# Kernel optimization log

Measured on AMD Instinct MI355X. Metric: run time of the kernel, lower is better.

Reference implementation:

```python
import jax, jax.numpy as jnp
import numpy as np
from jax import lax

STRIDE = 1
PADDING = 4
Q = 5


def setup_inputs() -> dict:
    key = jax.random.key(0)
    k1, k2, k3 = jax.random.split(key, 3)
    B, C_in, T = 16, 128, 8192
    C_out, K = 256, 9
    x = jax.random.normal(k1, (B, C_in, T), dtype=jnp.float32)
    fan_in = C_in * K
    std = np.sqrt(2.0 / fan_in).astype(np.float32)
    conv_weights = jax.random.normal(k2, (C_out, C_in, K, Q), dtype=jnp.float32) * std
    # init matches _initialize_weights' operator_probs pattern plus small noise
    operator_probs = jnp.concatenate(
        [jnp.full((C_out, 1), 1.5), jnp.full((C_out, Q - 1), 0.25)], axis=1
    ) + 0.01 * jax.random.normal(k3, (C_out, Q), dtype=jnp.float32)
    return {"x": x, "conv_weights": conv_weights, "operator_probs": operator_probs}


def _selfonn_forward(x, conv_weights, operator_probs):
    # Fuse the q parallel convs into one conv with q*C_out output channels.
    C_out, C_in, K, q = conv_weights.shape
    # (O, I, K, q) -> (q, O, I, K) -> (q*O, I, K); q-major output channel order
    w = jnp.transpose(conv_weights, (3, 0, 1, 2)).reshape(q * C_out, C_in, K)
    z = lax.conv_general_dilated(
        x, w,
        window_strides=(STRIDE,),
        padding=[(PADDING, PADDING)],
        dimension_numbers=("NCH", "OIH", "NCH"),
    )  # (B, q*C_out, T_out)
    B = x.shape[0]
    T_out = z.shape[-1]
    z = z.reshape(B, q, C_out, T_out)
    # per-branch nonlinearities: identity, sin, cos, tanh, clamped exp
    outs = jnp.stack(
        [
            z[:, 0],
            jnp.sin(z[:, 1]),
            jnp.cos(z[:, 2]),
            jnp.tanh(z[:, 3]),
            jnp.exp(jnp.clip(z[:, 4], -8.0, 8.0)),
        ],
        axis=-1,
    )  # (B, C_out, T_out, q)
    op_w = jax.nn.softmax(operator_probs, axis=1)  # (C_out, q)
    return jnp.einsum("bctq,cq->bct", outs, op_w)


def reference(x, conv_weights, operator_probs):
    return _selfonn_forward(x, conv_weights, operator_probs)
```

## Files before the change

### kernel.cpp

```cpp
#include <hip/hip_runtime.h>

#define CI   128
#define TT   8192
#define CO   256
#define KW   9
#define NQ   5
#define PADL 4
#define KDIM (CI*KW)
#define NSTEP (KDIM/32)
#define NCHUNK (NSTEP/2)
#define NF (NQ*NCHUNK)
#define BCO  128
#define BT   128
#define XROWS 136
#define XPITCH 136

typedef __attribute__((ext_vector_type(8))) short short8;
typedef __attribute__((ext_vector_type(4))) float float4v;
typedef __attribute__((address_space(1))) const unsigned int ga_u32;
typedef __attribute__((address_space(3))) unsigned int la_u32;

static __device__ __forceinline__ short f2bf(float f) {
  union { float f; unsigned u; } c; c.f = f;
  unsigned u = c.u;
  unsigned r = (u + 0x7FFFu + ((u >> 16) & 1u)) >> 16;
  return (short)r;
}

static __device__ __forceinline__ float tanh_fast(float z) {
  float e = __expf(2.f * z);
  return (e - 1.f) / (e + 1.f);
}

static __device__ __forceinline__ void gload_lds16(const void* g, void* l) {
  __builtin_amdgcn_global_load_lds((ga_u32*)g, (la_u32*)l, 16, 0, 0);
}

__global__ void selfonn_wtrans(const float* __restrict__ w, short* __restrict__ wT, int n) {
  int o = blockIdx.x * 256 + threadIdx.x;
  if (o >= n) return;
  int ci = o & (CI - 1);
  int k  = (o >> 7) % KW;
  int co = (o / KDIM) & (CO - 1);
  int q  = o / (KDIM * CO);
  wT[o] = f2bf(w[((co * CI + ci) * KW + k) * NQ + q]);
}

__global__ __launch_bounds__(256, 2) void selfonn_main(
    const float* __restrict__ x, const short* __restrict__ wT,
    const float* __restrict__ probs, float* __restrict__ out) {

  __shared__ __align__(16) short xs[XROWS][XPITCH];
  __shared__ __align__(16) short ws[2][2][BCO][32];
  __shared__ float opw[BCO][NQ];

  const int tid  = threadIdx.x;
  const int lane = tid & 63;
  const int wid  = tid >> 6;
  const int wm   = wid >> 1;
  const int wn   = wid & 1;
  const int l15  = lane & 15;
  const int lg   = lane >> 4;
  const int b    = blockIdx.z;
  const int co0  = blockIdx.y * BCO;
  const int t0   = blockIdx.x * BT;

  if (tid < BCO) {
    float p[NQ];
    float mx = -1e30f;
    #pragma unroll
    for (int j = 0; j < NQ; ++j) { p[j] = probs[(co0 + tid) * NQ + j]; mx = fmaxf(mx, p[j]); }
    float s = 0.f;
    #pragma unroll
    for (int j = 0; j < NQ; ++j) { p[j] = __expf(p[j] - mx); s += p[j]; }
    float inv = 1.0f / s;
    #pragma unroll
    for (int j = 0; j < NQ; ++j) opw[tid][j] = p[j] * inv;
  }

  const float* xb = x + (size_t)b * CI * TT;
  #pragma unroll
  for (int it = 0; it < 17; ++it) {
    int cell = tid + it * 256;
    int ci = cell & (CI - 1);
    int tc = cell >> 7;
    int tg = t0 - PADL + tc * 4;
    float4v v = {0.f, 0.f, 0.f, 0.f};
    if (tg >= 0 && tg <= TT - 4)
      v = *(const float4v*)(xb + (size_t)ci * TT + tg);
    int tl = tc * 4;
    xs[tl + 0][ci] = f2bf(v[0]);
    xs[tl + 1][ci] = f2bf(v[1]);
    xs[tl + 2][ci] = f2bf(v[2]);
    xs[tl + 3][ci] = f2bf(v[3]);
  }

  auto stage = [&](int fi, int buf) {
    int q     = fi / NCHUNK;
    int chunk = fi - q * NCHUNK;
    const short* wqp = wT + ((size_t)q * CO + co0) * KDIM + chunk * 64;
    short* lb = &ws[buf][0][0][0];
    #pragma unroll
    for (int r = 0; r < 4; ++r) {
      int idx_l = r * 256 + tid;
      int sc    = idx_l >> 9;
      int rem   = idx_l & 511;
      int co_l  = rem >> 2;
      int part  = rem & 3;
      const short* src = wqp + (size_t)co_l * KDIM + sc * 32 + part * 8;
      gload_lds16(src, lb + (size_t)(r * 256 + wid * 64) * 8);
    }
  };

  float4v oacc[4][4];
  float4v acc[4][4];
  #pragma unroll
  for (int m = 0; m < 4; ++m)
    #pragma unroll
    for (int n = 0; n < 4; ++n) {
      oacc[m][n] = (float4v){0.f, 0.f, 0.f, 0.f};
      acc[m][n]  = (float4v){0.f, 0.f, 0.f, 0.f};
    }

  stage(0, 0);
  __syncthreads();

  int cur = 0;
  for (int fi = 0; fi < NF; ++fi) {
    if (fi + 1 < NF) stage(fi + 1, cur ^ 1);

    int q     = fi / NCHUNK;
    int chunk = fi - q * NCHUNK;

    #pragma unroll
    for (int sc = 0; sc < 2; ++sc) {
      int step = chunk * 2 + sc;
      int k    = step >> 2;
      int ci0  = (step & 3) * 32;
      short8 af[4], bfv[4];
      #pragma unroll
      for (int m = 0; m < 4; ++m)
        af[m] = *(const short8*)&ws[cur][sc][wm * 64 + m * 16 + l15][8 * lg];
      #pragma unroll
      for (int n = 0; n < 4; ++n)
        bfv[n] = *(const short8*)&xs[wn * 64 + n * 16 + l15 + k][ci0 + 8 * lg];
      #pragma unroll
      for (int m = 0; m < 4; ++m)
        #pragma unroll
        for (int n = 0; n < 4; ++n)
          acc[m][n] = __builtin_amdgcn_mfma_f32_16x16x32_bf16(af[m], bfv[n], acc[m][n], 0, 0, 0);
    }

    if (chunk == NCHUNK - 1) {
      #define DO_EPI(FEXPR)                                            \
        _Pragma("unroll") for (int m = 0; m < 4; ++m) {                \
          _Pragma("unroll") for (int jj = 0; jj < 4; ++jj) {           \
            int co_l = wm * 64 + m * 16 + lg * 4 + jj;                 \
            float wqv = opw[co_l][q];                                  \
            _Pragma("unroll") for (int n = 0; n < 4; ++n) {            \
              float z = acc[m][n][jj];                                 \
              float f = (FEXPR);                                       \
              oacc[m][n][jj] += wqv * f;                               \
              acc[m][n][jj] = 0.f;                                     \
            }                                                          \
          }                                                            \
        }
      if (q == 0)      { DO_EPI(z) }
      else if (q == 1) { DO_EPI(__sinf(z)) }
      else if (q == 2) { DO_EPI(__cosf(z)) }
      else if (q == 3) { DO_EPI(tanh_fast(z)) }
      else             { DO_EPI(__expf(fminf(fmaxf(z, -8.f), 8.f))) }
      #undef DO_EPI
    }

    __syncthreads();
    cur ^= 1;
  }

  float* ob = out + (size_t)(b * CO + co0) * TT;
  #pragma unroll
  for (int m = 0; m < 4; ++m) {
    #pragma unroll
    for (int jj = 0; jj < 4; ++jj) {
      int co_l = wm * 64 + m * 16 + lg * 4 + jj;
      int tcol = t0 + wn * 64 + l15;
      float* orow = ob + (size_t)co_l * TT + tcol;
      #pragma unroll
      for (int n = 0; n < 4; ++n)
        orow[n * 16] = oacc[m][n][jj];
    }
  }
}

extern "C" void kernel_launch(void* const* d_in, const int* in_sizes, int n_in,
                              void* d_out, int out_size, void* d_ws, size_t ws_size,
                              hipStream_t stream) {
  const float* x     = (const float*)d_in[0];
  const float* w     = (const float*)d_in[1];
  const float* probs = (const float*)d_in[2];
  float* out = (float*)d_out;
  short* wT  = (short*)d_ws;

  int nw = NQ * CO * KDIM;
  selfonn_wtrans<<<dim3((nw + 255) / 256), 256, 0, stream>>>(w, wT, nw);

  dim3 grid(TT / BT, CO / BCO, 16);
  selfonn_main<<<grid, 256, 0, stream>>>(x, wT, probs, out);
}
```

Before: 418.1 us.

## Triple-buffer weight tiles with explicit vmcnt waits and swizzled LDS reads

Replaces the double-buffered two-substep weight staging with a three-deep ring of single-step weight tiles prefetched two iterations ahead. Explicit s_waitcnt vmcnt and raw s_barrier replace __syncthreads, so outstanding global-to-LDS loads can stay in flight across barriers. It also adds an XOR-style swizzle on the weight LDS addresses to cut bank conflicts, precomputes LDS offsets, and raises wave priority around the MFMA block. Hand-managed waitcnt values add a risk of races if the compiler emits extra vector memory ops, and the swizzle must match between the stage and read mappings.

```diff
diff --git a/kernel.cpp b/kernel.cpp
--- a/kernel.cpp
+++ b/kernel.cpp
@@ -7,13 +7,13 @@
 #define NQ   5
 #define PADL 4
 #define KDIM (CI*KW)
-#define NSTEP (KDIM/32)
-#define NCHUNK (NSTEP/2)
-#define NF (NQ*NCHUNK)
+#define NSTEP 36
+#define NF (NQ*NSTEP)
 #define BCO  128
 #define BT   128
 #define XROWS 136
 #define XPITCH 136
+#define WBUF_SHORTS (BCO*32)
 
 typedef __attribute__((ext_vector_type(8))) short short8;
 typedef __attribute__((ext_vector_type(4))) float float4v;
@@ -23,8 +23,7 @@
 static __device__ __forceinline__ short f2bf(float f) {
   union { float f; unsigned u; } c; c.f = f;
   unsigned u = c.u;
-  unsigned r = (u + 0x7FFFu + ((u >> 16) & 1u)) >> 16;
-  return (short)r;
+  return (short)((u + 0x7FFFu + ((u >> 16) & 1u)) >> 16);
 }
 
 static __device__ __forceinline__ float tanh_fast(float z) {
@@ -32,7 +31,7 @@
   return (e - 1.f) / (e + 1.f);
 }
 
-static __device__ __forceinline__ void gload_lds16(const void* g, void* l) {
+static __device__ __forceinline__ void gload_lds16(const short* g, short* l) {
   __builtin_amdgcn_global_load_lds((ga_u32*)g, (la_u32*)l, 16, 0, 0);
 }
 
@@ -51,7 +50,7 @@
     const float* __restrict__ probs, float* __restrict__ out) {
 
   __shared__ __align__(16) short xs[XROWS][XPITCH];
-  __shared__ __align__(16) short ws[2][2][BCO][32];
+  __shared__ __align__(16) short ws[3][WBUF_SHORTS];
   __shared__ float opw[BCO][NQ];
 
   const int tid  = threadIdx.x;
@@ -95,22 +94,26 @@
     xs[tl + 3][ci] = f2bf(v[3]);
   }
 
-  auto stage = [&](int fi, int buf) {
-    int q     = fi / NCHUNK;
-    int chunk = fi - q * NCHUNK;
-    const short* wqp = wT + ((size_t)q * CO + co0) * KDIM + chunk * 64;
-    short* lb = &ws[buf][0][0][0];
-    #pragma unroll
-    for (int r = 0; r < 4; ++r) {
-      int idx_l = r * 256 + tid;
-      int sc    = idx_l >> 9;
-      int rem   = idx_l & 511;
-      int co_l  = rem >> 2;
-      int part  = rem & 3;
-      const short* src = wqp + (size_t)co_l * KDIM + sc * 32 + part * 8;
-      gload_lds16(src, lb + (size_t)(r * 256 + wid * 64) * 8);
-    }
-  };
+  int soff[2];
+  #pragma unroll
+  for (int r = 0; r < 2; ++r) {
+    int G = r * 256 + tid;
+    int co_l = G >> 2;
+    int lgs  = (G - (G >> 3)) & 3;
+    soff[r] = co_l * KDIM + lgs * 8;
+  }
+  const int sdst0 = (wid * 64) * 8;
+  const int sdst1 = (256 + wid * 64) * 8;
+
+  int afo[4], bfo[4];
+  #pragma unroll
+  for (int m = 0; m < 4; ++m)
+    afo[m] = (wm * 64 + m * 16 + l15) * 32 + (((lg + (l15 >> 1)) & 3) << 3);
+  #pragma unroll
+  for (int n = 0; n < 4; ++n)
+    bfo[n] = (wn * 64 + n * 16 + l15) * XPITCH + (lg << 3);
+
+  const short* wq0 = wT + (size_t)co0 * KDIM;
 
   float4v oacc[4][4];
   float4v acc[4][4];
@@ -122,36 +125,53 @@
       acc[m][n]  = (float4v){0.f, 0.f, 0.f, 0.f};
     }
 
-  stage(0, 0);
+  gload_lds16(wq0 + soff[0],      &ws[0][0] + sdst0);
+  gload_lds16(wq0 + soff[1],      &ws[0][0] + sdst1);
+  gload_lds16(wq0 + soff[0] + 32, &ws[1][0] + sdst0);
+  gload_lds16(wq0 + soff[1] + 32, &ws[1][0] + sdst1);
   __syncthreads();
 
-  int cur = 0;
+  int cb = 0, sb = 2;
+  int s_step = 2, s_qoff = 0;
+  int q = 0, step = 0;
+
   for (int fi = 0; fi < NF; ++fi) {
-    if (fi + 1 < NF) stage(fi + 1, cur ^ 1);
-
-    int q     = fi / NCHUNK;
-    int chunk = fi - q * NCHUNK;
-
-    #pragma unroll
-    for (int sc = 0; sc < 2; ++sc) {
-      int step = chunk * 2 + sc;
-      int k    = step >> 2;
-      int ci0  = (step & 3) * 32;
-      short8 af[4], bfv[4];
-      #pragma unroll
-      for (int m = 0; m < 4; ++m)
-        af[m] = *(const short8*)&ws[cur][sc][wm * 64 + m * 16 + l15][8 * lg];
+    if (fi + 2 < NF) {
+      const short* wp = wq0 + s_qoff + s_step * 32;
+      short* lb = &ws[sb][0];
+      gload_lds16(wp + soff[0], lb + sdst0);
+      gload_lds16(wp + soff[1], lb + sdst1);
+      if (++s_step == NSTEP) { s_step = 0; s_qoff += CO * KDIM; }
+      asm volatile("s_waitcnt vmcnt(4)" ::: "memory");
+    } else if (fi + 2 == NF) {
+      asm volatile("s_waitcnt vmcnt(2)" ::: "memory");
+    } else {
+      asm volatile("s_waitcnt vmcnt(0)" ::: "memory");
+    }
+    __builtin_amdgcn_s_barrier();
+    __builtin_amdgcn_sched_barrier(0);
+
+    const short* wb = &ws[cb][0];
+    const int k   = step >> 2;
+    const int ci0 = (step & 3) << 5;
+    const int bsh = k * XPITCH + ci0;
+    short8 af[4], bfv[4];
+    #pragma unroll
+    for (int m = 0; m < 4; ++m)
+      af[m] = *(const short8*)(wb + afo[m]);
+    #pragma unroll
+    for (int n = 0; n < 4; ++n)
+      bfv[n] = *(const short8*)(&xs[0][0] + bfo[n] + bsh);
+
+    __builtin_amdgcn_s_setprio(1);
+    #pragma unroll
+    for (int m = 0; m < 4; ++m)
       #pragma unroll
       for (int n = 0; n < 4; ++n)
-        bfv[n] = *(const short8*)&xs[wn * 64 + n * 16 + l15 + k][ci0 + 8 * lg];
-      #pragma unroll
-      for (int m = 0; m < 4; ++m)
-        #pragma unroll
-        for (int n = 0; n < 4; ++n)
-          acc[m][n] = __builtin_amdgcn_mfma_f32_16x16x32_bf16(af[m], bfv[n], acc[m][n], 0, 0, 0);
-    }
-
-    if (chunk == NCHUNK - 1) {
+        acc[m][n] = __builtin_amdgcn_mfma_f32_16x16x32_bf16(af[m], bfv[n], acc[m][n], 0, 0, 0);
+    __builtin_amdgcn_s_setprio(0);
+
+    if (step == NSTEP - 1) {
       #define DO_EPI(FEXPR)                                            \
         _Pragma("unroll") for (int m = 0; m < 4; ++m) {                \
           _Pragma("unroll") for (int jj = 0; jj < 4; ++jj) {           \
@@ -172,9 +192,11 @@
       else             { DO_EPI(__expf(fminf(fmaxf(z, -8.f), 8.f))) }
       #undef DO_EPI
     }
-
-    __syncthreads();
-    cur ^= 1;
+    __builtin_amdgcn_s_barrier();
+
+    if (++step == NSTEP) { step = 0; ++q; }
+    cb = (cb == 2) ? 0 : cb + 1;
+    sb = (sb == 2) ? 0 : sb + 1;
   }
 
   float* ob = out + (size_t)(b * CO + co0) * TT;
```

Result: slower. 462.6 us (+10.6%).

## Deepen weight pipeline to 5-slot ring with register double-buffering and 512-thread tiles

Applied to the files above, without the earlier changes.

Doubles the time tile to 256 and uses 512 threads (8 waves), so each block reuses its staged weights across more outputs. Weight staging moves to a 5-slot LDS ring fed by async global-to-LDS loads issued four steps ahead, with explicit vmcnt waits and bare s_barrier instead of __syncthreads. MFMA fragments are double-buffered in registers, the weight layout in LDS gets an XOR-style swizzle to cut bank conflicts, and s_setprio wraps the MFMA block. The risks are higher register and LDS pressure, which may lower occupancy, and fragile manual wait counts.

```diff
diff --git a/kernel.cpp b/kernel.cpp
--- a/kernel.cpp
+++ b/kernel.cpp
@@ -7,13 +7,14 @@
 #define NQ   5
 #define PADL 4
 #define KDIM (CI*KW)
-#define NSTEP (KDIM/32)
-#define NCHUNK (NSTEP/2)
-#define NF (NQ*NCHUNK)
+#define NSTEP 36
+#define NF (NQ*NSTEP)
 #define BCO  128
-#define BT   128
-#define XROWS 136
+#define BT   256
+#define XROWS 264
 #define XPITCH 136
+#define WRING 5
+#define WSLOT (BCO*32)
 
 typedef __attribute__((ext_vector_type(8))) short short8;
 typedef __attribute__((ext_vector_type(4))) float float4v;
@@ -23,8 +24,7 @@
 static __device__ __forceinline__ short f2bf(float f) {
   union { float f; unsigned u; } c; c.f = f;
   unsigned u = c.u;
-  unsigned r = (u + 0x7FFFu + ((u >> 16) & 1u)) >> 16;
-  return (short)r;
+  return (short)((u + 0x7FFFu + ((u >> 16) & 1u)) >> 16);
 }
 
 static __device__ __forceinline__ float tanh_fast(float z) {
@@ -32,7 +32,7 @@
   return (e - 1.f) / (e + 1.f);
 }
 
-static __device__ __forceinline__ void gload_lds16(const void* g, void* l) {
+static __device__ __forceinline__ void gload_lds16(const short* g, short* l) {
   __builtin_amdgcn_global_load_lds((ga_u32*)g, (la_u32*)l, 16, 0, 0);
 }
 
@@ -46,19 +46,19 @@
   wT[o] = f2bf(w[((co * CI + ci) * KW + k) * NQ + q]);
 }
 
-__global__ __launch_bounds__(256, 2) void selfonn_main(
+__global__ __launch_bounds__(512, 2) void selfonn_main(
     const float* __restrict__ x, const short* __restrict__ wT,
     const float* __restrict__ probs, float* __restrict__ out) {
 
   __shared__ __align__(16) short xs[XROWS][XPITCH];
-  __shared__ __align__(16) short ws[2][2][BCO][32];
+  __shared__ __align__(16) short ws[WRING][WSLOT];
   __shared__ float opw[BCO][NQ];
 
   const int tid  = threadIdx.x;
   const int lane = tid & 63;
   const int wid  = tid >> 6;
-  const int wm   = wid >> 1;
-  const int wn   = wid & 1;
+  const int wm   = wid >> 2;
+  const int wt   = wid & 3;
   const int l15  = lane & 15;
   const int lg   = lane >> 4;
   const int b    = blockIdx.z;
@@ -78,39 +78,41 @@
     for (int j = 0; j < NQ; ++j) opw[tid][j] = p[j] * inv;
   }
 
+  const int soff = (tid >> 2) * KDIM + (((tid - (tid >> 3)) & 3) << 3);
+  const int sdst = wid * 512;
+  const short* wTb = wT + (size_t)co0 * KDIM;
+
+  #pragma unroll
+  for (int ps = 0; ps < 4; ++ps)
+    gload_lds16(wTb + ps * 32 + soff, &ws[ps][0] + sdst);
+
   const float* xb = x + (size_t)b * CI * TT;
-  #pragma unroll
   for (int it = 0; it < 17; ++it) {
-    int cell = tid + it * 256;
-    int ci = cell & (CI - 1);
-    int tc = cell >> 7;
-    int tg = t0 - PADL + tc * 4;
-    float4v v = {0.f, 0.f, 0.f, 0.f};
-    if (tg >= 0 && tg <= TT - 4)
-      v = *(const float4v*)(xb + (size_t)ci * TT + tg);
-    int tl = tc * 4;
-    xs[tl + 0][ci] = f2bf(v[0]);
-    xs[tl + 1][ci] = f2bf(v[1]);
-    xs[tl + 2][ci] = f2bf(v[2]);
-    xs[tl + 3][ci] = f2bf(v[3]);
-  }
-
-  auto stage = [&](int fi, int buf) {
-    int q     = fi / NCHUNK;
-    int chunk = fi - q * NCHUNK;
-    const short* wqp = wT + ((size_t)q * CO + co0) * KDIM + chunk * 64;
-    short* lb = &ws[buf][0][0][0];
-    #pragma unroll
-    for (int r = 0; r < 4; ++r) {
-      int idx_l = r * 256 + tid;
-      int sc    = idx_l >> 9;
-      int rem   = idx_l & 511;
-      int co_l  = rem >> 2;
-      int part  = rem & 3;
-      const short* src = wqp + (size_t)co_l * KDIM + sc * 32 + part * 8;
-      gload_lds16(src, lb + (size_t)(r * 256 + wid * 64) * 8);
-    }
-  };
+    int cell = tid + it * 512;
+    if (cell < XROWS / 4 * CI) {
+      int ci = cell & (CI - 1);
+      int tc = cell >> 7;
+      int tg = t0 - PADL + tc * 4;
+      float4v v = {0.f, 0.f, 0.f, 0.f};
+      if (tg >= 0 && tg <= TT - 4)
+        v = *(const float4v*)(xb + (size_t)ci * TT + tg);
+      int tl = tc * 4;
+      xs[tl + 0][ci] = f2bf(v[0]);
+      xs[tl + 1][ci] = f2bf(v[1]);
+      xs[tl + 2][ci] = f2bf(v[2]);
+      xs[tl + 3][ci] = f2bf(v[3]);
+    }
+  }
+
+  int afo[4], bfo[4];
+  #pragma unroll
+  for (int m = 0; m < 4; ++m) {
+    int co = wm * 64 + m * 16 + l15;
+    afo[m] = co * 32 + (((lg + (co >> 1)) & 3) << 3);
+  }
+  #pragma unroll
+  for (int n = 0; n < 4; ++n)
+    bfo[n] = (wt * 64 + n * 16 + l15) * XPITCH + (lg << 3);
 
   float4v oacc[4][4];
   float4v acc[4][4];
@@ -122,60 +124,78 @@
       acc[m][n]  = (float4v){0.f, 0.f, 0.f, 0.f};
     }
 
-  stage(0, 0);
   __syncthreads();
 
-  int cur = 0;
-  for (int fi = 0; fi < NF; ++fi) {
-    if (fi + 1 < NF) stage(fi + 1, cur ^ 1);
-
-    int q     = fi / NCHUNK;
-    int chunk = fi - q * NCHUNK;
-
-    #pragma unroll
-    for (int sc = 0; sc < 2; ++sc) {
-      int step = chunk * 2 + sc;
-      int k    = step >> 2;
-      int ci0  = (step & 3) * 32;
-      short8 af[4], bfv[4];
-      #pragma unroll
-      for (int m = 0; m < 4; ++m)
-        af[m] = *(const short8*)&ws[cur][sc][wm * 64 + m * 16 + l15][8 * lg];
-      #pragma unroll
-      for (int n = 0; n < 4; ++n)
-        bfv[n] = *(const short8*)&xs[wn * 64 + n * 16 + l15 + k][ci0 + 8 * lg];
-      #pragma unroll
-      for (int m = 0; m < 4; ++m)
-        #pragma unroll
-        for (int n = 0; n < 4; ++n)
-          acc[m][n] = __builtin_amdgcn_mfma_f32_16x16x32_bf16(af[m], bfv[n], acc[m][n], 0, 0, 0);
-    }
-
-    if (chunk == NCHUNK - 1) {
-      #define DO_EPI(FEXPR)                                            \
+  short8 frA_a[4], frA_b[4], frB_a[4], frB_b[4];
+  #pragma unroll
+  for (int m = 0; m < 4; ++m) frA_a[m] = *(const short8*)(&ws[0][0] + afo[m]);
+  #pragma unroll
+  for (int n = 0; n < 4; ++n) frA_b[n] = *(const short8*)(&xs[0][0] + bfo[n]);
+
+  int q = 0, sq = 0;
+  int rn = 1, rs = 4, kg = 4;
+  size_t woff = 4 * 32;
+
+  #define BODY(S, CA, CB, NA, NB)                                      \
+    {                                                                  \
+      const int s_ = (S);                                              \
+      if (s_ + 4 < NF) {                                               \
+        gload_lds16(wTb + woff + soff, &ws[rs][0] + sdst);             \
+        woff += 32;                                                    \
+        if (++kg == NSTEP) { kg = 0; woff += (size_t)(CO - 1) * KDIM; }\
+        rs = (rs == WRING - 1) ? 0 : rs + 1;                           \
+      }                                                                \
+                       \
+      {                                                                \
+        int sqn = (sq == NSTEP - 1) ? 0 : sq + 1;                      \
+        int bshn = (sqn >> 2) * XPITCH + ((sqn & 3) << 5);             \
+        const short* nb = &ws[rn][0];                                  \
+        _Pragma("unroll") for (int m = 0; m < 4; ++m)                  \
+          NA[m] = *(const short8*)(nb + afo[m]);                       \
+        const short* xp = &xs[0][0] + bshn;                            \
+        _Pragma("unroll") for (int n = 0; n < 4; ++n)                  \
+          NB[n] = *(const short8*)(xp + bfo[n]);                       \
+      }                                                                \
+      __builtin_amdgcn_s_setprio(1);                                   \
+      _Pragma("unroll") for (int m = 0; m < 4; ++m)                    \
+        _Pragma("unroll") for (int n = 0; n < 4; ++n)                  \
+          acc[m][n] = __builtin_amdgcn_mfma_f32_16x16x32_bf16(         \
+              CA[m], CB[n], acc[m][n], 0, 0, 0);                       \
+      __builtin_amdgcn_s_setprio(0);                                   \
+      if (sq == NSTEP - 1) {                                           \
         _Pragma("unroll") for (int m = 0; m < 4; ++m) {                \
           _Pragma("unroll") for (int jj = 0; jj < 4; ++jj) {           \
             int co_l = wm * 64 + m * 16 + lg * 4 + jj;                 \
             float wqv = opw[co_l][q];                                  \
             _Pragma("unroll") for (int n = 0; n < 4; ++n) {            \
               float z = acc[m][n][jj];                                 \
-              float f = (FEXPR);                                       \
+              float f;                                                 \
+              if (q == 0)      f = z;                                  \
+              else if (q == 1) f = __sinf(z);                          \
+              else if (q == 2) f = __cosf(z);                          \
+              else if (q == 3) f = tanh_fast(z);                       \
+              else             f = __expf(fminf(fmaxf(z, -8.f), 8.f)); \
               oacc[m][n][jj] += wqv * f;                               \
               acc[m][n][jj] = 0.f;                                     \
             }                                                          \
           }                                                            \
-        }
-      if (q == 0)      { DO_EPI(z) }
-      else if (q == 1) { DO_EPI(__sinf(z)) }
-      else if (q == 2) { DO_EPI(__cosf(z)) }
-      else if (q == 3) { DO_EPI(tanh_fast(z)) }
-      else             { DO_EPI(__expf(fminf(fmaxf(z, -8.f), 8.f))) }
-      #undef DO_EPI
-    }
-
-    __syncthreads();
-    cur ^= 1;
-  }
+        }                                                              \
+        ++q;                                                           \
+      }                                                                \
+      sq = (sq == NSTEP - 1) ? 0 : sq + 1;                             \
+      rn = (rn == WRING - 1) ? 0 : rn + 1;                             \
+      if (s_ + 4 < NF)       asm volatile("s_waitcnt vmcnt(2)" ::: "memory"); \
+      else if (s_ + 4 == NF) asm volatile("s_waitcnt vmcnt(1)" ::: "memory"); \
+      else                   asm volatile("s_waitcnt vmcnt(0)" ::: "memory"); \
+      __builtin_amdgcn_s_barrier();                                    \
+      asm volatile("" ::: "memory");                                   \
+    }
+
+  for (int s = 0; s < NF; s += 2) {
+    BODY(s,     frA_a, frA_b, frB_a, frB_b)
+    BODY(s + 1, frB_a, frB_b, frA_a, frA_b)
+  }
+  #undef BODY
 
   float* ob = out + (size_t)(b * CO + co0) * TT;
   #pragma unroll
@@ -183,7 +203,7 @@
     #pragma unroll
     for (int jj = 0; jj < 4; ++jj) {
       int co_l = wm * 64 + m * 16 + lg * 4 + jj;
-      int tcol = t0 + wn * 64 + l15;
+      int tcol = t0 + wt * 64 + l15;
       float* orow = ob + (size_t)co_l * TT + tcol;
       #pragma unroll
       for (int n = 0; n < 4; ++n)
@@ -205,5 +225,5 @@
   selfonn_wtrans<<<dim3((nw + 255) / 256), 256, 0, stream>>>(w, wT, nw);
 
   dim3 grid(TT / BT, CO / BCO, 16);
-  selfonn_main<<<grid, 256, 0, stream>>>(x, wT, probs, out);
-}
+  selfonn_main<<<grid, 512, 0, stream>>>(x, wT, probs, out);
+}
```

New measurement: 552.3 us. 1.32x slower.
